# Kernel optimization log

Measured on AMD Instinct MI355X. Metric: run time of the kernel, lower is better.

Reference implementation:

```python
import jax, jax.numpy as jnp
import numpy as np
import math

B, H, S, D = 2, 8, 512, 64

def setup_inputs() -> dict:
    key0 = jax.random.key(0)
    k1, k2, k3, k4, k5 = jax.random.split(key0, 5)
    return {
        "query": jax.random.normal(k1, (B, H, S, D), dtype=jnp.float32),
        "key":   jax.random.normal(k2, (B, H, S, D), dtype=jnp.float32),
        "value": jax.random.normal(k3, (B, H, S, D), dtype=jnp.float32),
        "R":     jax.random.normal(k4, (B, H, S, S, D), dtype=jnp.float32),
        "mask":  jax.random.randint(k5, (B, 1, S, S), 0, 2, dtype=jnp.int32),
    }

def reference(query, key, value, R, mask):
    d = query.shape[-1]
    # QK: [B,H,S,S]
    QK = jnp.einsum('bhqd,bhkd->bhqk', query, key)
    # QR: query . R per (q,k) pair -> [B,H,S,S]
    QR = jnp.einsum('bhqd,bhqkd->bhqk', query, R)
    scores = (QK + QR) / math.sqrt(d)
    neg = jnp.asarray(-1e9, scores.dtype)
    scores = jnp.where(mask == 0, neg, scores)
    p_attn = jax.nn.softmax(scores, axis=-1)
    p_attn = jnp.where(mask == 0, jnp.asarray(0.0, p_attn.dtype), p_attn)
    out = jnp.einsum('bhqk,bhkd->bhqd', p_attn, value)
    return out, p_attn
```

## Files before the change

### kernel.cpp

```cpp
#include <hip/hip_runtime.h>
#include <math.h>

#define Bb 2
#define Hh 8
#define Ss 512
#define Dd 64

typedef float floatx4 __attribute__((ext_vector_type(4)));

__global__ __launch_bounds__(256) void relattn_kernel(
    const float* __restrict__ Q, const float* __restrict__ Kmat,
    const float* __restrict__ V, const float* __restrict__ R,
    const int* __restrict__ mask, float* __restrict__ out,
    float* __restrict__ p_out)
{
    __shared__ float sq[Dd];
    __shared__ float ssc[Ss];
    __shared__ float sred[8];

    const int row = blockIdx.x;
    const int q   = row & (Ss - 1);
    const int bh  = row >> 9;
    const int b   = bh >> 3;
    const int tid = threadIdx.x;

    if (tid < Dd) sq[tid] = Q[(size_t)row * Dd + tid];
    __syncthreads();

    const int j  = tid & 15;
    const int kg = tid >> 4;
    const floatx4 qv = *(const floatx4*)&sq[j * 4];
    const float* Rrow = R    + (size_t)row * Ss * Dd;
    const float* Kbh  = Kmat + (size_t)bh  * Ss * Dd;

    for (int k = kg; k < Ss; k += 16) {
        floatx4 rv = __builtin_nontemporal_load(
            (const floatx4*)(Rrow + k * Dd + j * 4));
        floatx4 kv = *(const floatx4*)(Kbh + k * Dd + j * 4);
        float p = qv.x * (rv.x + kv.x) + qv.y * (rv.y + kv.y)
                + qv.z * (rv.z + kv.z) + qv.w * (rv.w + kv.w);
        p += __shfl_xor(p, 1);
        p += __shfl_xor(p, 2);
        p += __shfl_xor(p, 4);
        p += __shfl_xor(p, 8);
        if (j == 0) ssc[k] = p * 0.125f;
    }
    __syncthreads();

    const int* mrow = mask + (size_t)(b * Ss + q) * Ss;
    float s0 = ssc[tid], s1 = ssc[tid + 256];
    const int m0 = mrow[tid], m1 = mrow[tid + 256];
    if (m0 == 0) s0 = -1e9f;
    if (m1 == 0) s1 = -1e9f;

    float mx = fmaxf(s0, s1);
    #pragma unroll
    for (int o = 1; o < 64; o <<= 1) mx = fmaxf(mx, __shfl_xor(mx, o));
    if ((tid & 63) == 0) sred[tid >> 6] = mx;
    __syncthreads();
    mx = fmaxf(fmaxf(sred[0], sred[1]), fmaxf(sred[2], sred[3]));

    float e0 = __expf(s0 - mx);
    float e1 = __expf(s1 - mx);
    float sm = e0 + e1;
    #pragma unroll
    for (int o = 1; o < 64; o <<= 1) sm += __shfl_xor(sm, o);
    if ((tid & 63) == 0) sred[4 + (tid >> 6)] = sm;
    __syncthreads();
    sm = sred[4] + sred[5] + sred[6] + sred[7];

    const float inv = 1.0f / sm;
    const float p0 = (m0 == 0) ? 0.0f : e0 * inv;
    const float p1 = (m1 == 0) ? 0.0f : e1 * inv;

    float* prow = p_out + (size_t)row * Ss;
    prow[tid]       = p0;
    prow[tid + 256] = p1;

    ssc[tid]       = p0;
    ssc[tid + 256] = p1;
    __syncthreads();

    const int d = tid & 63;
    const int c = tid >> 6;
    const float* Vbh = V + (size_t)bh * Ss * Dd;
    float acc = 0.0f;
    #pragma unroll 4
    for (int k = c * 128; k < c * 128 + 128; ++k)
        acc = fmaf(ssc[k], Vbh[k * Dd + d], acc);

    __syncthreads();
    ssc[tid] = acc;
    __syncthreads();
    if (tid < 64) {
        float r = ssc[tid] + ssc[64 + tid] + ssc[128 + tid] + ssc[192 + tid];
        out[(size_t)row * Dd + tid] = r;
    }
}

extern "C" void kernel_launch(void* const* d_in, const int* in_sizes, int n_in,
                              void* d_out, int out_size, void* d_ws, size_t ws_size,
                              hipStream_t stream) {
    const float* Q    = (const float*)d_in[0];
    const float* K    = (const float*)d_in[1];
    const float* V    = (const float*)d_in[2];
    const float* R    = (const float*)d_in[3];
    const int*   mask = (const int*)d_in[4];

    float* out   = (float*)d_out;
    float* p_out = out + (size_t)Bb * Hh * Ss * Dd;

    relattn_kernel<<<Bb * Hh * Ss, 256, 0, stream>>>(Q, K, V, R, mask, out, p_out);
}
```

Measured before the change: 1.385 ms.

## Assign one query row per wavefront and replace block barriers with wave-local reductions

Each 256-thread block now handles four query rows, one per 64-lane wavefront, instead of one row per block. Block-wide __syncthreads and shared-memory reductions are replaced by wave barriers and shuffle reductions. The PV product now uses float4 loads of V with a cross-lane shuffle reduction. This removes block synchronisation overhead and cuts block count, but each wave streams a whole R row alone, which may limit memory-level parallelism per row.

```diff
diff --git a/kernel.cpp b/kernel.cpp
--- a/kernel.cpp
+++ b/kernel.cpp
@@ -14,26 +14,28 @@
     const int* __restrict__ mask, float* __restrict__ out,
     float* __restrict__ p_out)
 {
-    __shared__ float sq[Dd];
-    __shared__ float ssc[Ss];
-    __shared__ float sred[8];
+    __shared__ float ssc_all[4][Ss];
 
-    const int row = blockIdx.x;
+    const int tid  = threadIdx.x;
+    const int wave = tid >> 6;
+    const int lane = tid & 63;
+    float* ssc = ssc_all[wave];
+
+    const int row = blockIdx.x * 4 + wave;
     const int q   = row & (Ss - 1);
     const int bh  = row >> 9;
     const int b   = bh >> 3;
-    const int tid = threadIdx.x;
 
-    if (tid < Dd) sq[tid] = Q[(size_t)row * Dd + tid];
-    __syncthreads();
+    const int j  = lane & 15;
+    const int kg = lane >> 4;
 
-    const int j  = tid & 15;
-    const int kg = tid >> 4;
-    const floatx4 qv = *(const floatx4*)&sq[j * 4];
+    const floatx4 qv = *(const floatx4*)(Q + (size_t)row * Dd + j * 4);
     const float* Rrow = R    + (size_t)row * Ss * Dd;
     const float* Kbh  = Kmat + (size_t)bh  * Ss * Dd;
+    const float* Vbh  = V    + (size_t)bh  * Ss * Dd;
 
-    for (int k = kg; k < Ss; k += 16) {
+    #pragma unroll 4
+    for (int k = kg; k < Ss; k += 4) {
         floatx4 rv = __builtin_nontemporal_load(
             (const floatx4*)(Rrow + k * Dd + j * 4));
         floatx4 kv = *(const floatx4*)(Kbh + k * Dd + j * 4);
@@ -45,57 +47,57 @@
         p += __shfl_xor(p, 8);
         if (j == 0) ssc[k] = p * 0.125f;
     }
-    __syncthreads();
+    __builtin_amdgcn_wave_barrier();
 
     const int* mrow = mask + (size_t)(b * Ss + q) * Ss;
-    float s0 = ssc[tid], s1 = ssc[tid + 256];
-    const int m0 = mrow[tid], m1 = mrow[tid + 256];
-    if (m0 == 0) s0 = -1e9f;
-    if (m1 == 0) s1 = -1e9f;
-
-    float mx = fmaxf(s0, s1);
+    float s[8]; int m[8];
+    #pragma unroll
+    for (int i = 0; i < 8; ++i) {
+        m[i] = mrow[lane + 64 * i];
+        s[i] = ssc[lane + 64 * i];
+        if (m[i] == 0) s[i] = -1e9f;
+    }
+    float mx = s[0];
+    #pragma unroll
+    for (int i = 1; i < 8; ++i) mx = fmaxf(mx, s[i]);
     #pragma unroll
     for (int o = 1; o < 64; o <<= 1) mx = fmaxf(mx, __shfl_xor(mx, o));
-    if ((tid & 63) == 0) sred[tid >> 6] = mx;
-    __syncthreads();
-    mx = fmaxf(fmaxf(sred[0], sred[1]), fmaxf(sred[2], sred[3]));
 
-    float e0 = __expf(s0 - mx);
-    float e1 = __expf(s1 - mx);
-    float sm = e0 + e1;
+    float e[8], sm = 0.0f;
+    #pragma unroll
+    for (int i = 0; i < 8; ++i) { e[i] = __expf(s[i] - mx); sm += e[i]; }
     #pragma unroll
     for (int o = 1; o < 64; o <<= 1) sm += __shfl_xor(sm, o);
-    if ((tid & 63) == 0) sred[4 + (tid >> 6)] = sm;
-    __syncthreads();
-    sm = sred[4] + sred[5] + sred[6] + sred[7];
-
     const float inv = 1.0f / sm;
-    const float p0 = (m0 == 0) ? 0.0f : e0 * inv;
-    const float p1 = (m1 == 0) ? 0.0f : e1 * inv;
 
     float* prow = p_out + (size_t)row * Ss;
-    prow[tid]       = p0;
-    prow[tid + 256] = p1;
+    #pragma unroll
+    for (int i = 0; i < 8; ++i) {
+        float p = (m[i] == 0) ? 0.0f : e[i] * inv;
+        prow[lane + 64 * i] = p;
+        ssc[lane + 64 * i]  = p;
+    }
+    __builtin_amdgcn_wave_barrier();
 
-    ssc[tid]       = p0;
-    ssc[tid + 256] = p1;
-    __syncthreads();
-
-    const int d = tid & 63;
-    const int c = tid >> 6;
-    const float* Vbh = V + (size_t)bh * Ss * Dd;
-    float acc = 0.0f;
+    floatx4 acc = {0.f, 0.f, 0.f, 0.f};
     #pragma unroll 4
-    for (int k = c * 128; k < c * 128 + 128; ++k)
-        acc = fmaf(ssc[k], Vbh[k * Dd + d], acc);
-
-    __syncthreads();
-    ssc[tid] = acc;
-    __syncthreads();
-    if (tid < 64) {
-        float r = ssc[tid] + ssc[64 + tid] + ssc[128 + tid] + ssc[192 + tid];
-        out[(size_t)row * Dd + tid] = r;
+    for (int k = kg; k < Ss; k += 4) {
+        float pk = ssc[k];
+        floatx4 vv = *(const floatx4*)(Vbh + k * Dd + j * 4);
+        acc.x = fmaf(pk, vv.x, acc.x);
+        acc.y = fmaf(pk, vv.y, acc.y);
+        acc.z = fmaf(pk, vv.z, acc.z);
+        acc.w = fmaf(pk, vv.w, acc.w);
     }
+    #pragma unroll
+    for (int o = 16; o <= 32; o <<= 1) {
+        acc.x += __shfl_xor(acc.x, o);
+        acc.y += __shfl_xor(acc.y, o);
+        acc.z += __shfl_xor(acc.z, o);
+        acc.w += __shfl_xor(acc.w, o);
+    }
+    if (kg == 0)
+        *(floatx4*)(out + (size_t)row * Dd + j * 4) = acc;
 }
 
 extern "C" void kernel_launch(void* const* d_in, const int* in_sizes, int n_in,
@@ -110,5 +112,5 @@
     float* out   = (float*)d_out;
     float* p_out = out + (size_t)Bb * Hh * Ss * Dd;
 
-    relattn_kernel<<<Bb * Hh * Ss, 256, 0, stream>>>(Q, K, V, R, mask, out, p_out);
+    relattn_kernel<<<(Bb * Hh * Ss) / 4, 256, 0, stream>>>(Q, K, V, R, mask, out, p_out);
 }
```

New measurement: 1.291 ms. -6.8%, faster.
